# Kernel optimization log

Hardware: AMD Instinct MI355X
Metric: run time of the kernel (lower is better)

Reference implementation:

```python
import jax, jax.numpy as jnp
import numpy as np

# EKV constants from Config
VT = 0.025
N_FACTOR = 1.5
VD = 0.5
ALPHA = 2e-06
BASE_TIA = 500000.0

KERNEL = 3
STRIDE = 1
PAD = 1


def _unfold(x, k, stride, pad):
    # torch.nn.functional.unfold: (N, C, H, W) -> (N, C*k*k, L), patch dims ordered (c, kh, kw)
    N, C, H, W = x.shape
    xp = jnp.pad(x, ((0, 0), (0, 0), (pad, pad), (pad, pad)))
    Ho = (H + 2 * pad - k) // stride + 1
    Wo = (W + 2 * pad - k) // stride + 1
    patches = []
    for i in range(k):
        for j in range(k):
            patches.append(xp[:, :, i:i + stride * Ho:stride, j:j + stride * Wo:stride])
    # (k*k, N, C, Ho, Wo) -> (N, C, k*k, Ho*Wo) -> (N, C*k*k, L)
    p = jnp.stack(patches, axis=2)  # (N, C, k*k, Ho, Wo)
    return p.reshape(N, C * k * k, Ho * Wo), Ho, Wo


def setup_inputs() -> dict:
    key = jax.random.key(0)
    k1, k2 = jax.random.split(key)
    x = jax.random.normal(k1, (4, 64, 32, 32), dtype=jnp.float32)
    # theta ~ Normal(2.5, 0.5), shape (out_channels, in_channels, k, k)
    theta = 2.5 + 0.5 * jax.random.normal(k2, (64, 64, 3, 3), dtype=jnp.float32)
    return {"x": x, "theta": theta}


def reference(x, theta):
    N, C, H, W = x.shape
    O = theta.shape[0]
    fan_in = C * KERNEL * KERNEL
    tia_gain = BASE_TIA / (fan_in ** 0.5)
    phi = 2 * N_FACTOR * VT

    x_unf, Ho, Wo = _unfold(x, KERNEL, STRIDE, PAD)      # (N, C*k*k, L)
    x_in = x_unf[:, None, :, :]                           # (N, 1, CKK, L)
    w_th = theta.reshape(1, O, -1, 1)                     # (1, O, CKK, 1)

    v_diff = x_in - w_th                                  # (N, O, CKK, L)
    f_term = jnp.square(jax.nn.softplus(v_diff / phi))
    r_term = jnp.square(jax.nn.softplus((v_diff - VD) / phi))
    i_syn = ALPHA * (f_term - r_term)
    out_current = jnp.sum(i_syn, axis=2)                  # (N, O, L)
    out_voltage = out_current * tia_gain
    return out_voltage.reshape(N, O, Ho, Wo)
```

## Files before the change

kernel.cpp:

```cpp
#include <hip/hip_runtime.h>
#include <math.h>

#define CIN 64
#define HH 32
#define WW 32
#define NW (64 * 64 * 9)
#define LUT_N 1024


__global__ __launch_bounds__(256) void prep_kernel(const float* __restrict__ theta,
                                                   float* __restrict__ ws) {
    constexpr float SZ = 19.235933878519512f;
    const int b = blockIdx.x;
    if (b < NW / 256) {
        int i = b * 256 + threadIdx.x;
        ws[i] = fmaf(theta[i], -16.0f * SZ, 512.0f);
    } else {
        const double D2 = 9.6179661929342026;
        float2* lut = (float2*)(ws + NW);
        for (int j = threadIdx.x; j < LUT_N; j += 256) {
            double z0 = -32.0 + j * 0.0625;
            double z1 = z0 + 0.0625;
            double f0 = log2(1.0 + exp2(z0)), f1 = log2(1.0 + exp2(z1));
            double r0 = log2(1.0 + exp2(z0 - D2)), r1 = log2(1.0 + exp2(z1 - D2));
            double g0 = f0 * f0 - r0 * r0;
            double g1 = f1 * f1 - r1 * r1;
            double S = g1 - g0;
            double B = g0 - S * (double)j;
            lut[j] = make_float2((float)S, (float)B);
        }
    }
}

__global__ __launch_bounds__(256) void ekv_kernel(
        const float* __restrict__ x, const float* __restrict__ ws,
        float* __restrict__ out) {
    constexpr float SZ16 = 16.0f * 19.235933878519512f;
    constexpr float OS = 0.020018875579925058f;

    __shared__ float2 lut[LUT_N];

    const int t = threadIdx.x;
    {
        const float2* lg = (const float2*)(ws + NW);
#pragma unroll
        for (int i = 0; i < LUT_N / 256; ++i)
            lut[t + 256 * i] = lg[t + 256 * i];
    }
    __syncthreads();

    const int wo = t & 31;
    const int hr = t >> 5;
    const int ho = (int)blockIdx.y * 8 + hr;
    const int n  = (int)blockIdx.z;
    const int o  = (int)blockIdx.x;

    const float* xb = x + n * (CIN * HH * WW);
    const float* W0 = ws + o * (CIN * 9);

    int   off[9];
    float m[9];
#pragma unroll
    for (int di = 0; di < 3; ++di) {
#pragma unroll
        for (int dj = 0; dj < 3; ++dj) {
            int h = ho + di - 1, w = wo + dj - 1;
            bool v = (h >= 0) && (h < HH) && (w >= 0) && (w < WW);
            int hc = min(max(h, 0), HH - 1);
            int wc = min(max(w, 0), WW - 1);
            off[di * 3 + dj] = hc * WW + wc;
            m[di * 3 + dj] = v ? SZ16 : 0.0f;
        }
    }

    float accS = 0.f, accB = 0.f;

#pragma unroll 2
    for (int c = 0; c < CIN; ++c) {
        const float* xc = xb + c * (HH * WW);
        float xv[9];
#pragma unroll
        for (int k = 0; k < 9; ++k) xv[k] = xc[off[k]];

        const float* Wc = W0 + c * 9;
#pragma unroll
        for (int k = 0; k < 9; ++k) {
            float tt = fmaf(xv[k], m[k], Wc[k]);
#if __has_builtin(__builtin_amdgcn_fmed3f)
            float tc = __builtin_amdgcn_fmed3f(tt, 0.0f, 1023.0f);
#else
            float tc = fminf(fmaxf(tt, 0.0f), 1023.0f);
#endif
            unsigned idx = (unsigned)tc;
            float2 sb = lut[idx];
            accS = fmaf(sb.x, tt, accS);
            accB += sb.y;
        }
    }

    out[((n * 64 + o) * HH + ho) * WW + wo] = (accS + accB) * OS;
}

extern "C" void kernel_launch(void* const* d_in, const int* in_sizes, int n_in,
                              void* d_out, int out_size, void* d_ws, size_t ws_size,
                              hipStream_t stream) {
    const float* x     = (const float*)d_in[0];
    const float* theta = (const float*)d_in[1];
    float* out = (float*)d_out;
    float* ws  = (float*)d_ws;

    prep_kernel<<<NW / 256 + 1, 256, 0, stream>>>(theta, ws);

    dim3 grid(64, 4, 4);
    dim3 block(256);
    ekv_kernel<<<grid, block, 0, stream>>>(x, ws, out);
}
```

Baseline: 90.57 us.

## Map output channels to lanes and skip taps below a per-tap threshold

Remaps the work so each wavefront handles one output pixel, with its 64 lanes covering the 64 output channels. A prep pass computes, for each (c,k) tap, the minimum theta over output channels minus a margin. At run time a wave ballot drops every tap whose scaled input is below that threshold for all channels, since those terms add only a tiny softplus-squared value. Weights are transposed so each lane reads coalesced weights. The inputs are also prefetched one channel ahead. The trade is a small bounded approximation error and divergent loop trip counts across waves.

```diff
diff --git a/kernel.cpp b/kernel.cpp
--- a/kernel.cpp
+++ b/kernel.cpp
@@ -4,29 +4,41 @@
 #define CIN 64
 #define HH 32
 #define WW 32
-#define NW (64 * 64 * 9)
+#define NO 64
+#define NCK (CIN * 9)
+#define NW  (NO * NCK)
 #define LUT_N 1024
 
+#define WS_TAU NW
+#define WS_LUT (NW + NCK)
+
+constexpr float SZf  = 19.235933878519512f;
+constexpr float SZ16 = 16.0f * 19.235933878519512f;
+constexpr float MARG = 8.0f / 19.235933878519512f;
 
 __global__ __launch_bounds__(256) void prep_kernel(const float* __restrict__ theta,
                                                    float* __restrict__ ws) {
-    constexpr float SZ = 19.235933878519512f;
-    const int b = blockIdx.x;
+    const int b = blockIdx.x, t = threadIdx.x;
     if (b < NW / 256) {
-        int i = b * 256 + threadIdx.x;
-        ws[i] = fmaf(theta[i], -16.0f * SZ, 512.0f);
+        int i = b * 256 + t;
+        int o = i & 63, ck = i >> 6;
+        ws[i] = fmaf(theta[o * NCK + ck], -SZ16, 512.0f);
+    } else if (b < NW / 256 + 3) {
+        int ck = (b - NW / 256) * 256 + t;
+        if (ck < NCK) {
+            float mn = 1e30f;
+            for (int o = 0; o < NO; ++o) mn = fminf(mn, theta[o * NCK + ck]);
+            ws[WS_TAU + ck] = (mn - MARG) * SZ16;
+        }
     } else {
         const double D2 = 9.6179661929342026;
-        float2* lut = (float2*)(ws + NW);
-        for (int j = threadIdx.x; j < LUT_N; j += 256) {
-            double z0 = -32.0 + j * 0.0625;
-            double z1 = z0 + 0.0625;
+        float2* lut = (float2*)(ws + WS_LUT);
+        for (int j = t; j < LUT_N; j += 256) {
+            double z0 = -32.0 + j * 0.0625, z1 = z0 + 0.0625;
             double f0 = log2(1.0 + exp2(z0)), f1 = log2(1.0 + exp2(z1));
             double r0 = log2(1.0 + exp2(z0 - D2)), r1 = log2(1.0 + exp2(z1 - D2));
-            double g0 = f0 * f0 - r0 * r0;
-            double g1 = f1 * f1 - r1 * r1;
-            double S = g1 - g0;
-            double B = g0 - S * (double)j;
+            double g0 = f0 * f0 - r0 * r0, g1 = f1 * f1 - r1 * r1;
+            double S = g1 - g0, B = g0 - S * (double)j;
             lut[j] = make_float2((float)S, (float)B);
         }
     }
@@ -35,70 +47,67 @@
 __global__ __launch_bounds__(256) void ekv_kernel(
         const float* __restrict__ x, const float* __restrict__ ws,
         float* __restrict__ out) {
-    constexpr float SZ16 = 16.0f * 19.235933878519512f;
     constexpr float OS = 0.020018875579925058f;
-
     __shared__ float2 lut[LUT_N];
 
     const int t = threadIdx.x;
     {
-        const float2* lg = (const float2*)(ws + NW);
+        const float2* lg = (const float2*)(ws + WS_LUT);
 #pragma unroll
-        for (int i = 0; i < LUT_N / 256; ++i)
-            lut[t + 256 * i] = lg[t + 256 * i];
+        for (int i = 0; i < LUT_N / 256; ++i) lut[t + 256 * i] = lg[t + 256 * i];
     }
     __syncthreads();
 
-    const int wo = t & 31;
-    const int hr = t >> 5;
-    const int ho = (int)blockIdx.y * 8 + hr;
-    const int n  = (int)blockIdx.z;
-    const int o  = (int)blockIdx.x;
+    const int lane = t & 63;
+    const int wv   = t >> 6;
+    const int pix  = (int)blockIdx.x * 4 + wv;
+    const int n  = pix >> 10;
+    const int ho = (pix >> 5) & 31;
+    const int wo = pix & 31;
 
-    const float* xb = x + n * (CIN * HH * WW);
-    const float* W0 = ws + o * (CIN * 9);
+    const int k9 = lane < 9 ? lane : 8;
+    const int di = k9 / 3, dj = k9 % 3;
+    const int h = ho + di - 1, w = wo + dj - 1;
+    const bool valid = (lane < 9) && (h >= 0) && (h < HH) && (w >= 0) && (w < WW);
+    const int hc = min(max(h, 0), HH - 1), wc = min(max(w, 0), WW - 1);
+    const float msc = valid ? SZ16 : 0.0f;
 
-    int   off[9];
-    float m[9];
-#pragma unroll
-    for (int di = 0; di < 3; ++di) {
-#pragma unroll
-        for (int dj = 0; dj < 3; ++dj) {
-            int h = ho + di - 1, w = wo + dj - 1;
-            bool v = (h >= 0) && (h < HH) && (w >= 0) && (w < WW);
-            int hc = min(max(h, 0), HH - 1);
-            int wc = min(max(w, 0), WW - 1);
-            off[di * 3 + dj] = hc * WW + wc;
-            m[di * 3 + dj] = v ? SZ16 : 0.0f;
-        }
-    }
+    const float* xptr = x + n * (CIN * HH * WW) + hc * WW + wc;
+    const float* tptr = ws + WS_TAU + k9;
 
     float accS = 0.f, accB = 0.f;
 
-#pragma unroll 2
+    float xv = xptr[0];
+    float tv = tptr[0];
+
     for (int c = 0; c < CIN; ++c) {
-        const float* xc = xb + c * (HH * WW);
-        float xv[9];
-#pragma unroll
-        for (int k = 0; k < 9; ++k) xv[k] = xc[off[k]];
+        const float* xpn = (c < CIN - 1) ? xptr + HH * WW : xptr;
+        const float* tpn = (c < CIN - 1) ? tptr + 9 : tptr;
+        float xvn = xpn[0];
+        float tvn = tpn[0];
+        xptr = xpn; tptr = tpn;
 
-        const float* Wc = W0 + c * 9;
-#pragma unroll
-        for (int k = 0; k < 9; ++k) {
-            float tt = fmaf(xv[k], m[k], Wc[k]);
-#if __has_builtin(__builtin_amdgcn_fmed3f)
+        float xs = xv * msc;
+        unsigned m = (unsigned)__ballot(xs >= tv) & 0x1FFu;
+        const int ckb = c * 9;
+        while (m) {
+            int k = __builtin_ctz(m);
+            m &= m - 1;
+            int ck = ckb + k;
+            float Wv = ws[(ck << 6) + lane];
+            int xbits = __builtin_amdgcn_readlane(__builtin_bit_cast(int, xs), k);
+            float sx = __builtin_bit_cast(float, xbits);
+            float tt = sx + Wv;
             float tc = __builtin_amdgcn_fmed3f(tt, 0.0f, 1023.0f);
-#else
-            float tc = fminf(fmaxf(tt, 0.0f), 1023.0f);
-#endif
             unsigned idx = (unsigned)tc;
             float2 sb = lut[idx];
             accS = fmaf(sb.x, tt, accS);
             accB += sb.y;
         }
+        xv = xvn; tv = tvn;
     }
 
-    out[((n * 64 + o) * HH + ho) * WW + wo] = (accS + accB) * OS;
+    out[((n * 64 + lane) * HH + ho) * WW + wo] = (accS + accB) * OS;
 }
 
 extern "C" void kernel_launch(void* const* d_in, const int* in_sizes, int n_in,
@@ -109,9 +118,7 @@
     float* out = (float*)d_out;
     float* ws  = (float*)d_ws;
 
-    prep_kernel<<<NW / 256 + 1, 256, 0, stream>>>(theta, ws);
+    prep_kernel<<<NW / 256 + 4, 256, 0, stream>>>(theta, ws);
 
-    dim3 grid(64, 4, 4);
-    dim3 block(256);
-    ekv_kernel<<<grid, block, 0, stream>>>(x, ws, out);
+    ekv_kernel<<<1024, 256, 0, stream>>>(x, ws, out);
 }
```

Result: slower. 105.6 us (+16.6%).
